# Kernel tuning notes

Hardware: AMD Instinct MI355X
Metric: run time of the kernel (lower is better)

The kernel has to match this reference:

```python
import jax, jax.numpy as jnp
import numpy as np

C, N, E = 256, 256, 2048          # subgraphs, nodes/subgraph, edges/subgraph
F_IN, NHID, DDI = 128, 128, 256
K1, K2, K3 = 128, 64, 32          # top-k sizes for pooling_ratio=0.5
P, B = 16, 16                     # DAG hierarchy: P parents x B leaf children
GN = C + P + 1                    # global DAG nodes (leaves + parents + root)
GE = 8192                         # global pos/neg edge count


def setup_inputs():
    key = jax.random.key(0)
    ks = jax.random.split(key, 16)
    inp = {
        "x": jax.random.normal(ks[0], (C, N, F_IN), jnp.float32),
        "edge_index": jax.random.randint(ks[1], (C, 2, E), 0, N),
        "edge_weight": jax.random.uniform(ks[2], (C, E), dtype=jnp.float32),
        "global_edge_index": jax.random.randint(ks[3], (2, GE), 0, GN),
        "neg_edge_index": jax.random.randint(ks[4], (2, GE), 0, GN),
    }
    names = [("W1", F_IN, NHID), ("Wp1", NHID, 1), ("W2", NHID, NHID),
             ("Wp2", NHID, 1), ("W3", NHID, NHID), ("Wp3", NHID, 1),
             ("Wg", 6 * NHID, DDI), ("Wl1", DDI, DDI), ("Wl2", DDI, DDI)]
    for i, (nm, fi, fo) in enumerate(names):
        inp[nm] = jax.random.normal(ks[5 + i], (fi, fo), jnp.float32) / np.sqrt(fi)
        inp["b" + nm[1:]] = jnp.zeros((fo,), jnp.float32)
    return inp


def gcn(x, ei, ew, W, b):
    """PyG GCNConv with self-loops: D^-1/2 (A+I) D^-1/2 X W + b."""
    n = x.shape[0]
    h = x @ W
    row, col = ei[0], ei[1]
    deg = 1.0 + jax.ops.segment_sum(ew, col, num_segments=n)
    dis = jax.lax.rsqrt(deg)
    norm = dis[row] * ew * dis[col]                       # [E]
    agg = jax.ops.segment_sum(norm[:, None] * h[row], col, num_segments=n)
    return agg + h / deg[:, None] + b


def sag_pool(x, ei, ew, Ws, bs, k):
    """SAGPooling: GCN score, per-graph top-k, gate by tanh(score), edge filter."""
    n = x.shape[0]
    score = gcn(x, ei, ew, Ws, bs)[:, 0]
    vals, perm = jax.lax.top_k(score, k)
    x_new = x[perm] * jnp.tanh(vals)[:, None]
    newid = jnp.full((n,), -1, jnp.int32).at[perm].set(jnp.arange(k, dtype=jnp.int32))
    r, c = newid[ei[0]], newid[ei[1]]
    keep = (r >= 0) & (c >= 0)
    ei_new = jnp.where(keep, jnp.stack([r, c]), 0)        # dropped edges -> node 0
    ew_new = jnp.where(keep, ew, 0.0)                     # with zero weight
    return x_new, ei_new, ew_new


def _subgraph(x, ei, ew, W1, b1, Wp1, bp1, W2, b2, Wp2, bp2, W3, b3, Wp3, bp3):
    x = jax.nn.relu(gcn(x, ei, ew, W1, b1))
    x, ei, ew = sag_pool(x, ei, ew, Wp1, bp1, K1)
    x1 = jnp.concatenate([x.max(0), x.mean(0)])           # gmp||gap, batch all-zero
    x = jax.nn.relu(gcn(x, ei, ew, W2, b2))
    x, ei, ew = sag_pool(x, ei, ew, Wp2, bp2, K2)
    x2 = jnp.concatenate([x.max(0), x.mean(0)])
    x = jax.nn.relu(gcn(x, ei, ew, W3, b3))
    x, ei, ew = sag_pool(x, ei, ew, Wp3, bp3, K3)
    x3 = jnp.concatenate([x.max(0), x.mean(0)])
    return jnp.concatenate([x1, x2, x3])                  # [6*NHID]


def reference(x, edge_index, edge_weight, global_edge_index, neg_edge_index,
              W1, b1, Wp1, bp1, W2, b2, Wp2, bp2, W3, b3, Wp3, bp3,
              Wg, bg, Wl1, bl1, Wl2, bl2):
    # per-class subgraph pipeline, vmapped over the C subgraphs
    leaf = jax.vmap(_subgraph, in_axes=(0, 0, 0) + (None,) * 12)(
        x, edge_index, edge_weight,
        W1, b1, Wp1, bp1, W2, b2, Wp2, bp2, W3, b3, Wp3, bp3)   # [C, 6*NHID]
    # Get_Fs: mean-aggregate children features up the DAG (fixed 2-level + root)
    parent = leaf.reshape(P, B, -1).mean(axis=1)                # [P, 6*NHID]
    root = parent.mean(axis=0, keepdims=True)                   # [1, 6*NHID]
    gfeat = jnp.concatenate([leaf, parent, root], axis=0)       # [GN, 6*NHID]
    # global GCN (unit edge weights)
    gx = jax.nn.relu(gcn(gfeat, global_edge_index,
                         jnp.ones((GE,), gfeat.dtype), Wg, bg)) # [GN, DDI]
    class_embedding = gx[:C]
    # feature_split + lin1/lin2 + dot-product scores
    pos_s = gx[global_edge_index[0]] @ Wl1 + bl1
    pos_t = gx[global_edge_index[1]] @ Wl2 + bl2
    neg_s = gx[neg_edge_index[0]] @ Wl1 + bl1
    neg_t = gx[neg_edge_index[1]] @ Wl2 + bl2
    pos = jnp.sum(pos_s * pos_t, axis=1)
    neg = jnp.sum(neg_s * neg_t, axis=1)
    # BCEWithLogits: targets 1 for pos, 0 for neg
    loss = jnp.mean(jax.nn.softplus(-pos)) + jnp.mean(jax.nn.softplus(neg))
    return class_embedding, loss
```

## Files before the change

kernel.cpp:

```cpp
#include <hip/hip_runtime.h>
#include <math.h>

#define NT 1024
#define EDGES 2048
#define SENT 0xFFFF

struct SmemA {
  float xbuf[256 * 128];
  unsigned short rc[EDGES];
  float ewl[EDGES];
  unsigned short csr_row[EDGES];
  float csr_coef[EDGES];
  float degs[256];
  float diss[256];
  int   csr_off[257];
  int   csr_cnt[256];
  float hsv[256];
  float scorev[256];
  float vals[128];
  short perm[128];
  signed char newid[256];
};

__device__ __forceinline__ float4* xvec(float* xb, int row, int c4) {
  return reinterpret_cast<float4*>(xb + (row << 7) + ((c4 ^ (row & 7)) << 2));
}
__device__ __forceinline__ int xidx(int row, int col) {
  return (row << 7) + ((((col >> 2) ^ (row & 7)) << 2) | (col & 3));
}

template<int NN, int K, bool FIRST, bool REMAP>
__device__ __forceinline__ void run_stage(
    SmemA& sm,
    const float* __restrict__ xg,
    const int* __restrict__ eic,
    const float* __restrict__ ewc,
    const float* __restrict__ W,
    const float* __restrict__ b,
    const float* __restrict__ Wp,
    const float* __restrict__ bp,
    float* __restrict__ leaf_out,
    float& lmax, float& lmean)
{
  constexpr int NPT  = NN / 64;
  constexpr int Q    = NN / 64;
  constexpr int SEG  = NT / NN;
  constexpr int LEN  = NN / SEG;
  constexpr int LOG  = (NN == 256) ? 8 : (NN == 128 ? 7 : 6);
  const int tid  = threadIdx.x;
  const int lane = tid & 63;
  const int fbase = __builtin_amdgcn_readfirstlane((tid >> 6) << 3);
  const int c4b   = fbase >> 2;

  if (FIRST) {
    if (tid < NN) { sm.degs[tid] = 1.0f; sm.csr_cnt[tid] = 0; }
    __syncthreads();
    const float4* xg4 = reinterpret_cast<const float4*>(xg);
    for (int i = tid; i < 256 * 32; i += NT) {
      const float4 v = xg4[i];
      *xvec(sm.xbuf, i >> 5, i & 31) = v;
    }
    for (int e = tid; e < EDGES; e += NT) {
      const int row = eic[e], col = eic[EDGES + e];
      const float w = ewc[e];
      sm.rc[e]  = (unsigned short)((row << 8) | col);
      sm.ewl[e] = w;
      atomicAdd(&sm.degs[col], w);
      atomicAdd(&sm.csr_cnt[col], 1);
    }
    __syncthreads();
  }

  if (tid < NN) sm.diss[tid] = rsqrtf(sm.degs[tid]);
  if (tid < 64) {
    int c[Q], pre[Q];
    int tot = 0;
#pragma unroll
    for (int i = 0; i < Q; i++) { c[i] = sm.csr_cnt[tid * Q + i]; pre[i] = tot; tot += c[i]; }
    int inc = tot;
#pragma unroll
    for (int d = 1; d < 64; d <<= 1) {
      const int o = __shfl_up(inc, d, 64);
      if (tid >= d) inc += o;
    }
    const int base = inc - tot;
    if (tid == 0) sm.csr_off[0] = 0;
#pragma unroll
    for (int i = 0; i < Q; i++) {
      sm.csr_off[tid * Q + i + 1] = base + pre[i] + c[i];
      sm.csr_cnt[tid * Q + i] = 0;
    }
  }
  __syncthreads();

  if (tid < NN) sm.hsv[tid] = 0.0f;
  for (int e = tid; e < EDGES; e += NT) {
    const unsigned short r = sm.rc[e];
    if (FIRST || r != SENT) {
      const int row = r >> 8, col = r & 255;
      const int p = atomicAdd(&sm.csr_cnt[col], 1);
      const int s = sm.csr_off[col] + p;
      sm.csr_row[s]  = (unsigned short)row;
      sm.csr_coef[s] = sm.diss[row] * sm.ewl[e];
    }
  }
  __syncthreads();

  float acc[NPT][8];
#pragma unroll
  for (int i = 0; i < NPT; i++)
#pragma unroll
    for (int j = 0; j < 8; j++) acc[i][j] = 0.0f;

#pragma unroll 4
  for (int k4 = 0; k4 < 32; k4++) {
    float4 xv[NPT];
#pragma unroll
    for (int i = 0; i < NPT; i++) xv[i] = *xvec(sm.xbuf, lane + (i << 6), k4);
#pragma unroll
    for (int kk = 0; kk < 4; kk++) {
      const float* wr = W + (((k4 << 2) + kk) << 7) + fbase;
      const float4 wa = *reinterpret_cast<const float4*>(wr);
      const float4 wb = *reinterpret_cast<const float4*>(wr + 4);
      const float wv[8] = {wa.x, wa.y, wa.z, wa.w, wb.x, wb.y, wb.z, wb.w};
#pragma unroll
      for (int i = 0; i < NPT; i++) {
        const float xs = (kk == 0) ? xv[i].x : (kk == 1) ? xv[i].y : (kk == 2) ? xv[i].z : xv[i].w;
#pragma unroll
        for (int j = 0; j < 8; j++) acc[i][j] = fmaf(xs, wv[j], acc[i][j]);
      }
    }
  }
  __syncthreads();

#pragma unroll
  for (int i = 0; i < NPT; i++) {
    const int v = lane + (i << 6);
    *xvec(sm.xbuf, v, c4b)     = make_float4(acc[i][0], acc[i][1], acc[i][2], acc[i][3]);
    *xvec(sm.xbuf, v, c4b + 1) = make_float4(acc[i][4], acc[i][5], acc[i][6], acc[i][7]);
  }
  __syncthreads();

  {
    const float4 ba = *reinterpret_cast<const float4*>(b + fbase);
    const float4 bb = *reinterpret_cast<const float4*>(b + fbase + 4);
    const float bv[8] = {ba.x, ba.y, ba.z, ba.w, bb.x, bb.y, bb.z, bb.w};
    const float4 wa = *reinterpret_cast<const float4*>(Wp + fbase);
    const float4 wb = *reinterpret_cast<const float4*>(Wp + fbase + 4);
    const float wv[8] = {wa.x, wa.y, wa.z, wa.w, wb.x, wb.y, wb.z, wb.w};
#pragma unroll
    for (int i = 0; i < NPT; i++) {
      const int v = lane + (i << 6);
      const int beg = sm.csr_off[v], end = sm.csr_off[v + 1];
      float ag[8] = {0.f, 0.f, 0.f, 0.f, 0.f, 0.f, 0.f, 0.f};
      float4 plo = make_float4(0.f, 0.f, 0.f, 0.f), phi = plo;
      float cf_nxt = 0.0f;
      if (beg < end) {
        const int r0 = sm.csr_row[beg];
        cf_nxt = sm.csr_coef[beg];
        plo = *xvec(sm.xbuf, r0, c4b);
        phi = *xvec(sm.xbuf, r0, c4b + 1);
      }
      for (int s = beg; s < end; ++s) {
        const float4 lo = plo, hi = phi;
        const float cf = cf_nxt;
        if (s + 1 < end) {
          const int rn = sm.csr_row[s + 1];
          cf_nxt = sm.csr_coef[s + 1];
          plo = *xvec(sm.xbuf, rn, c4b);
          phi = *xvec(sm.xbuf, rn, c4b + 1);
        }
        ag[0] = fmaf(cf, lo.x, ag[0]); ag[1] = fmaf(cf, lo.y, ag[1]);
        ag[2] = fmaf(cf, lo.z, ag[2]); ag[3] = fmaf(cf, lo.w, ag[3]);
        ag[4] = fmaf(cf, hi.x, ag[4]); ag[5] = fmaf(cf, hi.y, ag[5]);
        ag[6] = fmaf(cf, hi.z, ag[6]); ag[7] = fmaf(cf, hi.w, ag[7]);
      }
      const float dv = sm.diss[v];
      const float invd = 1.0f / sm.degs[v];
      float part = 0.0f;
#pragma unroll
      for (int j = 0; j < 8; j++) {
        acc[i][j] = fmaxf(fmaf(ag[j], dv, fmaf(acc[i][j], invd, bv[j])), 0.0f);
        part = fmaf(acc[i][j], wv[j], part);
      }
      atomicAdd(&sm.hsv[v], part);
    }
  }
  __syncthreads();

#pragma unroll
  for (int i = 0; i < NPT; i++) {
    const int v = lane + (i << 6);
    *xvec(sm.xbuf, v, c4b)     = make_float4(acc[i][0], acc[i][1], acc[i][2], acc[i][3]);
    *xvec(sm.xbuf, v, c4b + 1) = make_float4(acc[i][4], acc[i][5], acc[i][6], acc[i][7]);
  }
  if (tid < NN) {
    const int v = tid;
    const int beg = sm.csr_off[v], end = sm.csr_off[v + 1];
    float s = 0.0f;
    int r_nxt = 0; float c_nxt = 0.0f;
    if (beg < end) { r_nxt = sm.csr_row[beg]; c_nxt = sm.csr_coef[beg]; }
    for (int e2 = beg; e2 < end; e2++) {
      const int r = r_nxt; const float cf = c_nxt;
      if (e2 + 1 < end) { r_nxt = sm.csr_row[e2 + 1]; c_nxt = sm.csr_coef[e2 + 1]; }
      s = fmaf(cf, sm.hsv[r], s);
    }
    sm.scorev[v] = s * sm.diss[v] + sm.hsv[v] / sm.degs[v] + bp[0];
    sm.csr_cnt[v] = 0;
  }
  __syncthreads();

  {
    const int node = tid & (NN - 1);
    const int seg  = tid >> LOG;
    const float sv = sm.scorev[node];
    int part = 0;
    const int u0 = seg * LEN;
#pragma unroll 4
    for (int u = u0; u < u0 + LEN; u++) {
      const float su = sm.scorev[u];
      part += (su > sv) || (su == sv && u < node);
    }
    if (part) atomicAdd(&sm.csr_cnt[node], part);
  }
  __syncthreads();
  if (tid < NN) {
    const int rank = sm.csr_cnt[tid];
    if (rank < K) { sm.perm[rank] = (short)tid; sm.vals[rank] = sm.scorev[tid]; sm.newid[tid] = (signed char)rank; }
    else sm.newid[tid] = -1;
    if (tid < K) { sm.degs[tid] = 1.0f; sm.csr_cnt[tid] = 0; }
  }
  __syncthreads();

  {
    constexpr int TPR = NT / K;
    constexpr int C4  = 32 / TPR;
    const int drow = tid / TPR;
    const int cc   = (tid % TPR) * C4;
    const int src  = sm.perm[drow];
    const float g  = tanhf(sm.vals[drow]);
    float4 tmp[C4];
#pragma unroll
    for (int j = 0; j < C4; j++) tmp[j] = *xvec(sm.xbuf, src, cc + j);
    __syncthreads();
#pragma unroll
    for (int j = 0; j < C4; j++) {
      tmp[j].x *= g; tmp[j].y *= g; tmp[j].z *= g; tmp[j].w *= g;
      *xvec(sm.xbuf, drow, cc + j) = tmp[j];
    }
  }
  __syncthreads();

  if (tid < 128) {
    float mx = -INFINITY, sv = 0.0f;
    for (int i = 0; i < K; i++) {
      const float v = sm.xbuf[xidx(i, tid)];
      mx = fmaxf(mx, v); sv += v;
    }
    lmax = mx;
    lmean = sv * (1.0f / K);
    leaf_out[tid] = mx;
    leaf_out[128 + tid] = lmean;
  }
  if (REMAP) {
    for (int e = tid; e < EDGES; e += NT) {
      const unsigned short r = sm.rc[e];
      if (FIRST || r != SENT) {
        const int r2 = sm.newid[r >> 8];
        const int c2 = sm.newid[r & 255];
        if (r2 < 0 || c2 < 0) sm.rc[e] = SENT;
        else {
          sm.rc[e] = (unsigned short)((r2 << 8) | c2);
          atomicAdd(&sm.degs[c2], sm.ewl[e]);
          atomicAdd(&sm.csr_cnt[c2], 1);
        }
      }
    }
  }
  __syncthreads();
}

__global__ __launch_bounds__(NT)
void stageA_kernel(const float* __restrict__ x0,
                   const int* __restrict__ ei, const float* __restrict__ ew,
                   const float* __restrict__ W1, const float* __restrict__ b1,
                   const float* __restrict__ Wp1, const float* __restrict__ bp1,
                   const float* __restrict__ W2, const float* __restrict__ b2,
                   const float* __restrict__ Wp2, const float* __restrict__ bp2,
                   const float* __restrict__ W3, const float* __restrict__ b3,
                   const float* __restrict__ Wp3, const float* __restrict__ bp3,
                   const float* __restrict__ Wg,
                   float* __restrict__ gfeat, float* __restrict__ hG)
{
  __shared__ SmemA sm;
  const int c = blockIdx.x;
  const int tid = threadIdx.x;
  if (c == 0 && tid < 256) hG[(size_t)272 * 256 + tid] = 0.0f;
  const int* eic = ei + (size_t)c * 2 * EDGES;
  const float* ewc = ew + (size_t)c * EDGES;
  const float* xgc = x0 + (size_t)c * 256 * 128;
  float* leaf = gfeat + (size_t)c * 768;
  float l0 = 0.f, l1 = 0.f, l2 = 0.f, l3 = 0.f, l4 = 0.f, l5 = 0.f;
  run_stage<256, 128, true,  true >(sm, xgc, eic, ewc, W1, b1, Wp1, bp1, leaf + 0,   l0, l1);
  run_stage<128,  64, false, true >(sm, nullptr, nullptr, nullptr, W2, b2, Wp2, bp2, leaf + 256, l2, l3);
  run_stage< 64,  32, false, false>(sm, nullptr, nullptr, nullptr, W3, b3, Wp3, bp3, leaf + 512, l4, l5);

  float* leafbuf = sm.csr_coef;
  float* hGacc   = sm.degs;
  if (tid < 256) {
    if (tid < 128) {
      leafbuf[tid]       = l0; leafbuf[128 + tid] = l1;
      leafbuf[256 + tid] = l2; leafbuf[384 + tid] = l3;
      leafbuf[512 + tid] = l4; leafbuf[640 + tid] = l5;
    }
    hGacc[tid] = 0.0f;
  }
  __syncthreads();
  {
    const int f = tid & 255, q = tid >> 8;
    const float* wgq = Wg + (size_t)(q * 192) * 256 + f;
    const float* lb  = leafbuf + q * 192;
    float p0 = 0.f, p1 = 0.f, p2 = 0.f, p3 = 0.f;
    for (int i = 0; i < 192; i += 4) {
      p0 = fmaf(lb[i],     wgq[(size_t)i * 256],       p0);
      p1 = fmaf(lb[i + 1], wgq[(size_t)(i + 1) * 256], p1);
      p2 = fmaf(lb[i + 2], wgq[(size_t)(i + 2) * 256], p2);
      p3 = fmaf(lb[i + 3], wgq[(size_t)(i + 3) * 256], p3);
    }
    atomicAdd(&hGacc[f], (p0 + p1) + (p2 + p3));
  }
  __syncthreads();
  if (tid < 256) hG[(size_t)c * 256 + tid] = hGacc[tid];
}

__global__ __launch_bounds__(NT)
void prep_k(const float* __restrict__ gfeat, const float* __restrict__ Wg,
            float* __restrict__ hG, const int* __restrict__ gei,
            float* __restrict__ degG, int* __restrict__ goff,
            int* __restrict__ gcsr_row, float* __restrict__ gcsr_coef,
            float* __restrict__ lacc, int* __restrict__ lctr) {
  const int tid = threadIdx.x;
  if (blockIdx.x == 16) {
    __shared__ int cnt[320];
    __shared__ int off[321];
    __shared__ int fc[288];
    for (int i = tid; i < 320; i += NT) cnt[i] = 0;
    if (tid < 288) fc[tid] = 0;
    __syncthreads();
    for (int e = tid; e < 8192; e += NT) atomicAdd(&cnt[gei[8192 + e]], 1);
    __syncthreads();
    if (tid < 64) {
      int c[5], pre[5];
      int tot = 0;
#pragma unroll
      for (int i = 0; i < 5; i++) { c[i] = cnt[tid * 5 + i]; pre[i] = tot; tot += c[i]; }
      int inc = tot;
#pragma unroll
      for (int d = 1; d < 64; d <<= 1) {
        const int o = __shfl_up(inc, d, 64);
        if (tid >= d) inc += o;
      }
      const int base = inc - tot;
      if (tid == 0) off[0] = 0;
#pragma unroll
      for (int i = 0; i < 5; i++) off[tid * 5 + i + 1] = base + pre[i] + c[i];
    }
    if (tid < 273) degG[tid] = 1.0f + (float)cnt[tid];
    __syncthreads();
    for (int e = tid; e < 8192; e += NT) {
      const int col = gei[8192 + e], row = gei[e];
      const int p = atomicAdd(&fc[col], 1);
      const int s = off[col] + p;
      gcsr_row[s]  = row;
      gcsr_coef[s] = rsqrtf(1.0f + (float)cnt[row]);
    }
    if (tid < 274) goff[tid] = off[tid];
    if (tid == 0) { *lacc = 0.0f; *lctr = 0; }
    return;
  }
  const int p = blockIdx.x;
  __shared__ float prow[768];
  __shared__ float hGacc[256];
  for (int k = tid; k < 768; k += NT) {
    float s0 = 0.f, s1 = 0.f;
#pragma unroll
    for (int b2 = 0; b2 < 16; b2 += 2) {
      s0 += gfeat[(size_t)(p * 16 + b2) * 768 + k];
      s1 += gfeat[(size_t)(p * 16 + b2 + 1) * 768 + k];
    }
    prow[k] = (s0 + s1) * (1.0f / 16.0f);
  }
  if (tid < 256) hGacc[tid] = 0.0f;
  __syncthreads();
  {
    const int f = tid & 255, q = tid >> 8;
    const float* wgq = Wg + (size_t)(q * 192) * 256 + f;
    const float* lb  = prow + q * 192;
    float p0 = 0.f, p1 = 0.f, p2 = 0.f, p3 = 0.f;
    for (int i = 0; i < 192; i += 4) {
      p0 = fmaf(lb[i],     wgq[(size_t)i * 256],       p0);
      p1 = fmaf(lb[i + 1], wgq[(size_t)(i + 1) * 256], p1);
      p2 = fmaf(lb[i + 2], wgq[(size_t)(i + 2) * 256], p2);
      p3 = fmaf(lb[i + 3], wgq[(size_t)(i + 3) * 256], p3);
    }
    atomicAdd(&hGacc[f], (p0 + p1) + (p2 + p3));
  }
  __syncthreads();
  if (tid < 256) {
    const float hv = hGacc[tid];
    hG[(size_t)(256 + p) * 256 + tid] = hv;
    atomicAdd(&hG[(size_t)272 * 256 + tid], hv * (1.0f / 16.0f));
  }
}

__global__ __launch_bounds__(NT)
void gaggemb_k(const float* __restrict__ hG, const float* __restrict__ degG,
               const int* __restrict__ goff, const int* __restrict__ gcsr_row,
               const float* __restrict__ gcsr_coef, const float* __restrict__ bg,
               const float* __restrict__ Wl1, const float* __restrict__ bl1,
               const float* __restrict__ Wl2, const float* __restrict__ bl2,
               float* __restrict__ out_ce, float* __restrict__ A,
               float* __restrict__ B) {
  __shared__ float pacc[1024];
  __shared__ float pacc2[1024];
  __shared__ float gxr[256];
  const int v = blockIdx.x, tid = threadIdx.x;
  const int f = tid & 255, q = tid >> 8;
  const int beg = goff[v], end = goff[v + 1];
  float s = 0.f;
  for (int i = beg + q; i < end; i += 4)
    s = fmaf(gcsr_coef[i], hG[(size_t)gcsr_row[i] * 256 + f], s);
  pacc[tid] = s;
  __syncthreads();
  if (tid < 256) {
    const float dg = degG[v];
    float val = (pacc[tid] + pacc[256 + tid] + pacc[512 + tid] + pacc[768 + tid]) * rsqrtf(dg)
              + hG[(size_t)v * 256 + tid] / dg + bg[tid];
    val = fmaxf(val, 0.0f);
    gxr[tid] = val;
    if (v < 256) out_ce[(size_t)v * 256 + tid] = val;
  }
  __syncthreads();
  {
    const int k0 = q << 6;
    float a = 0.f, b2 = 0.f;
    for (int k = k0; k < k0 + 64; k++) {
      const float g = gxr[k];
      a  = fmaf(g, Wl1[(size_t)k * 256 + f], a);
      b2 = fmaf(g, Wl2[(size_t)k * 256 + f], b2);
    }
    pacc[tid] = a; pacc2[tid] = b2;
  }
  __syncthreads();
  if (tid < 256) {
    A[(size_t)v * 256 + tid] = pacc[tid] + pacc[256 + tid] + pacc[512 + tid] + pacc[768 + tid] + bl1[tid];
    B[(size_t)v * 256 + tid] = pacc2[tid] + pacc2[256 + tid] + pacc2[512 + tid] + pacc2[768 + tid] + bl2[tid];
  }
}

__global__ __launch_bounds__(256)
void loss_k(const float* __restrict__ A, const float* __restrict__ B,
            const int* __restrict__ gei, const int* __restrict__ nei,
            float* __restrict__ acc, int* __restrict__ lctr,
            float* __restrict__ out) {
  const int gw = (blockIdx.x * blockDim.x + threadIdx.x) >> 6;
  const int lane = threadIdx.x & 63;
  float lsum = 0.0f;
  for (int idx = gw; idx < 16384; idx += 512) {
    const bool ispos = idx < 8192;
    const int e = ispos ? idx : idx - 8192;
    const int* ia = ispos ? gei : nei;
    const int s = ia[e], t = ia[8192 + e];
    float p = 0.0f;
#pragma unroll
    for (int j = 0; j < 4; j++)
      p += A[(size_t)s * 256 + lane + 64 * j] * B[(size_t)t * 256 + lane + 64 * j];
#pragma unroll
    for (int off = 32; off; off >>= 1) p += __shfl_xor(p, off, 64);
    const float z = ispos ? -p : p;
    lsum += fmaxf(z, 0.0f) + log1pf(expf(-fabsf(z)));
  }
  if (lane == 0) atomicAdd(acc, lsum);
  __syncthreads();
  if (threadIdx.x == 0) {
    __threadfence();
    const int old = atomicAdd(lctr, 1);
    if (old == (int)gridDim.x - 1) {
      const float tot = atomicAdd(acc, 0.0f);
      out[65536] = tot * (1.0f / 8192.0f);
    }
  }
}

extern "C" void kernel_launch(void* const* d_in, const int* in_sizes, int n_in,
                              void* d_out, int out_size, void* d_ws, size_t ws_size,
                              hipStream_t stream) {
  const float* x   = (const float*)d_in[0];
  const int*   ei  = (const int*)d_in[1];
  const float* ew  = (const float*)d_in[2];
  const int*   gei = (const int*)d_in[3];
  const int*   nei = (const int*)d_in[4];
  const float* W1  = (const float*)d_in[5];
  const float* b1  = (const float*)d_in[6];
  const float* Wp1 = (const float*)d_in[7];
  const float* bp1 = (const float*)d_in[8];
  const float* W2  = (const float*)d_in[9];
  const float* b2  = (const float*)d_in[10];
  const float* Wp2 = (const float*)d_in[11];
  const float* bp2 = (const float*)d_in[12];
  const float* W3  = (const float*)d_in[13];
  const float* b3  = (const float*)d_in[14];
  const float* Wp3 = (const float*)d_in[15];
  const float* bp3 = (const float*)d_in[16];
  const float* Wg  = (const float*)d_in[17];
  const float* bg  = (const float*)d_in[18];
  const float* Wl1 = (const float*)d_in[19];
  const float* bl1 = (const float*)d_in[20];
  const float* Wl2 = (const float*)d_in[21];
  const float* bl2 = (const float*)d_in[22];

  float* ws       = (float*)d_ws;
  float* gfeat    = ws;
  float* hG       = gfeat + 256 * 768;
  float* degG     = hG + 273 * 256;
  float* Aemb     = degG + 288;
  float* Bemb     = Aemb + 273 * 256;
  float* lacc     = Bemb + 273 * 256;
  int*   lctr     = (int*)(lacc + 1);
  int*   goff     = lctr + 1;
  int*   gcsr_row = goff + 288;
  float* gcsr_coef= (float*)(gcsr_row + 8192);
  float* out      = (float*)d_out;

  stageA_kernel<<<256, NT, 0, stream>>>(x, ei, ew, W1, b1, Wp1, bp1,
                                        W2, b2, Wp2, bp2, W3, b3, Wp3, bp3,
                                        Wg, gfeat, hG);
  prep_k<<<17, NT, 0, stream>>>(gfeat, Wg, hG, gei, degG, goff,
                                gcsr_row, gcsr_coef, lacc, lctr);
  gaggemb_k<<<273, NT, 0, stream>>>(hG, degG, goff, gcsr_row, gcsr_coef, bg,
                                    Wl1, bl1, Wl2, bl2, out, Aemb, Bemb);
  loss_k<<<128, 256, 0, stream>>>(Aemb, Bemb, gei, nei, lacc, lctr, out);
}
```

Measured before the change: 185.8 us.

## Fuse global GCN tail into one cooperative kernel and compute parents from hG

```diff
diff --git a/kernel.cpp b/kernel.cpp
--- a/kernel.cpp
+++ b/kernel.cpp
@@ -1,9 +1,12 @@
 #include <hip/hip_runtime.h>
+#include <hip/hip_cooperative_groups.h>
 #include <math.h>
 
 #define NT 1024
 #define EDGES 2048
 #define SENT 0xFFFF
+
+namespace cg = cooperative_groups;
 
 struct SmemA {
   float xbuf[256 * 128];
@@ -39,7 +42,6 @@
     const float* __restrict__ b,
     const float* __restrict__ Wp,
     const float* __restrict__ bp,
-    float* __restrict__ leaf_out,
     float& lmax, float& lmean)
 {
   constexpr int NPT  = NN / 64;
@@ -93,7 +95,7 @@
   }
   __syncthreads();
 
-  if (tid < NN) sm.hsv[tid] = 0.0f;
+  if (tid < NN) { sm.hsv[tid] = 0.0f; sm.scorev[tid] = 0.0f; }
   for (int e = tid; e < EDGES; e += NT) {
     const unsigned short r = sm.rc[e];
     if (FIRST || r != SENT) {
@@ -194,19 +196,17 @@
     *xvec(sm.xbuf, v, c4b)     = make_float4(acc[i][0], acc[i][1], acc[i][2], acc[i][3]);
     *xvec(sm.xbuf, v, c4b + 1) = make_float4(acc[i][4], acc[i][5], acc[i][6], acc[i][7]);
   }
+  for (int e = tid; e < EDGES; e += NT) {
+    const unsigned short r = sm.rc[e];
+    if (FIRST || r != SENT) {
+      const int row = r >> 8, col = r & 255;
+      atomicAdd(&sm.scorev[col], sm.diss[row] * sm.ewl[e] * sm.hsv[row]);
+    }
+  }
+  __syncthreads();
   if (tid < NN) {
-    const int v = tid;
-    const int beg = sm.csr_off[v], end = sm.csr_off[v + 1];
-    float s = 0.0f;
-    int r_nxt = 0; float c_nxt = 0.0f;
-    if (beg < end) { r_nxt = sm.csr_row[beg]; c_nxt = sm.csr_coef[beg]; }
-    for (int e2 = beg; e2 < end; e2++) {
-      const int r = r_nxt; const float cf = c_nxt;
-      if (e2 + 1 < end) { r_nxt = sm.csr_row[e2 + 1]; c_nxt = sm.csr_coef[e2 + 1]; }
-      s = fmaf(cf, sm.hsv[r], s);
-    }
-    sm.scorev[v] = s * sm.diss[v] + sm.hsv[v] / sm.degs[v] + bp[0];
-    sm.csr_cnt[v] = 0;
+    sm.scorev[tid] = sm.scorev[tid] * sm.diss[tid] + sm.hsv[tid] / sm.degs[tid] + bp[0];
+    sm.csr_cnt[tid] = 0;
   }
   __syncthreads();
 
@@ -259,8 +259,6 @@
     }
     lmax = mx;
     lmean = sv * (1.0f / K);
-    leaf_out[tid] = mx;
-    leaf_out[128 + tid] = lmean;
   }
   if (REMAP) {
     for (int e = tid; e < EDGES; e += NT) {
@@ -289,21 +287,18 @@
                    const float* __restrict__ Wp2, const float* __restrict__ bp2,
                    const float* __restrict__ W3, const float* __restrict__ b3,
                    const float* __restrict__ Wp3, const float* __restrict__ bp3,
-                   const float* __restrict__ Wg,
-                   float* __restrict__ gfeat, float* __restrict__ hG)
+                   const float* __restrict__ Wg, float* __restrict__ hG)
 {
   __shared__ SmemA sm;
   const int c = blockIdx.x;
   const int tid = threadIdx.x;
-  if (c == 0 && tid < 256) hG[(size_t)272 * 256 + tid] = 0.0f;
   const int* eic = ei + (size_t)c * 2 * EDGES;
   const float* ewc = ew + (size_t)c * EDGES;
   const float* xgc = x0 + (size_t)c * 256 * 128;
-  float* leaf = gfeat + (size_t)c * 768;
   float l0 = 0.f, l1 = 0.f, l2 = 0.f, l3 = 0.f, l4 = 0.f, l5 = 0.f;
-  run_stage<256, 128, true,  true >(sm, xgc, eic, ewc, W1, b1, Wp1, bp1, leaf + 0,   l0, l1);
-  run_stage<128,  64, false, true >(sm, nullptr, nullptr, nullptr, W2, b2, Wp2, bp2, leaf + 256, l2, l3);
-  run_stage< 64,  32, false, false>(sm, nullptr, nullptr, nullptr, W3, b3, Wp3, bp3, leaf + 512, l4, l5);
+  run_stage<256, 128, true,  true >(sm, xgc, eic, ewc, W1, b1, Wp1, bp1, l0, l1);
+  run_stage<128,  64, false, true >(sm, nullptr, nullptr, nullptr, W2, b2, Wp2, bp2, l2, l3);
+  run_stage< 64,  32, false, false>(sm, nullptr, nullptr, nullptr, W3, b3, Wp3, bp3, l4, l5);
 
   float* leafbuf = sm.csr_coef;
   float* hGacc   = sm.degs;
@@ -333,27 +328,56 @@
   if (tid < 256) hG[(size_t)c * 256 + tid] = hGacc[tid];
 }
 
-__global__ __launch_bounds__(NT)
-void prep_k(const float* __restrict__ gfeat, const float* __restrict__ Wg,
-            float* __restrict__ hG, const int* __restrict__ gei,
+struct TailSm {
+  float pacc[1024];
+  float pacc2[1024];
+  float gxr[256];
+};
+
+__global__ __launch_bounds__(NT, 1)
+void tail_k(float* __restrict__ hG, const int* __restrict__ gei,
+            const int* __restrict__ nei, const float* __restrict__ bg,
+            const float* __restrict__ Wl1, const float* __restrict__ bl1,
+            const float* __restrict__ Wl2, const float* __restrict__ bl2,
             float* __restrict__ degG, int* __restrict__ goff,
             int* __restrict__ gcsr_row, float* __restrict__ gcsr_coef,
-            float* __restrict__ lacc, int* __restrict__ lctr) {
-  const int tid = threadIdx.x;
-  if (blockIdx.x == 16) {
-    __shared__ int cnt[320];
-    __shared__ int off[321];
-    __shared__ int fc[288];
+            float* __restrict__ A, float* __restrict__ B,
+            float* __restrict__ lacc, int* __restrict__ lctr,
+            float* __restrict__ out)
+{
+  __shared__ TailSm ts;
+  cg::grid_group grid = cg::this_grid();
+  const int c = blockIdx.x, tid = threadIdx.x;
+
+  if (c == 0) {
+    for (int w = tid; w < 16 * 256; w += NT) {
+      const int p = w >> 8, f = w & 255;
+      float s = 0.f;
+#pragma unroll
+      for (int b2 = 0; b2 < 16; b2++) s += hG[(size_t)(p * 16 + b2) * 256 + f];
+      hG[(size_t)(256 + p) * 256 + f] = s * (1.0f / 16.0f);
+    }
+    __syncthreads();
+    if (tid < 256) {
+      float s = 0.f;
+#pragma unroll
+      for (int p = 0; p < 16; p++) s += hG[(size_t)(256 + p) * 256 + tid];
+      hG[(size_t)272 * 256 + tid] = s * (1.0f / 16.0f);
+    }
+  } else if (c == 1) {
+    int* cnt = (int*)ts.pacc;
+    int* off = (int*)ts.pacc + 320;
+    int* fc  = (int*)ts.pacc + 644;
     for (int i = tid; i < 320; i += NT) cnt[i] = 0;
     if (tid < 288) fc[tid] = 0;
     __syncthreads();
     for (int e = tid; e < 8192; e += NT) atomicAdd(&cnt[gei[8192 + e]], 1);
     __syncthreads();
     if (tid < 64) {
-      int c[5], pre[5];
+      int cc[5], pre[5];
       int tot = 0;
 #pragma unroll
-      for (int i = 0; i < 5; i++) { c[i] = cnt[tid * 5 + i]; pre[i] = tot; tot += c[i]; }
+      for (int i = 0; i < 5; i++) { cc[i] = cnt[tid * 5 + i]; pre[i] = tot; tot += cc[i]; }
       int inc = tot;
 #pragma unroll
       for (int d = 1; d < 64; d <<= 1) {
@@ -363,7 +387,7 @@
       const int base = inc - tot;
       if (tid == 0) off[0] = 0;
 #pragma unroll
-      for (int i = 0; i < 5; i++) off[tid * 5 + i + 1] = base + pre[i] + c[i];
+      for (int i = 0; i < 5; i++) off[tid * 5 + i + 1] = base + pre[i] + cc[i];
     }
     if (tid < 273) degG[tid] = 1.0f + (float)cnt[tid];
     __syncthreads();
@@ -376,118 +400,79 @@
     }
     if (tid < 274) goff[tid] = off[tid];
     if (tid == 0) { *lacc = 0.0f; *lctr = 0; }
-    return;
-  }
-  const int p = blockIdx.x;
-  __shared__ float prow[768];
-  __shared__ float hGacc[256];
-  for (int k = tid; k < 768; k += NT) {
-    float s0 = 0.f, s1 = 0.f;
-#pragma unroll
-    for (int b2 = 0; b2 < 16; b2 += 2) {
-      s0 += gfeat[(size_t)(p * 16 + b2) * 768 + k];
-      s1 += gfeat[(size_t)(p * 16 + b2 + 1) * 768 + k];
-    }
-    prow[k] = (s0 + s1) * (1.0f / 16.0f);
-  }
-  if (tid < 256) hGacc[tid] = 0.0f;
-  __syncthreads();
+  }
+  grid.sync();
+
+  for (int rr = 0; rr < 2; rr++) {
+    if (rr == 1 && c >= 17) break;
+    const int v = rr ? 256 + c : c;
+    const int f = tid & 255, q = tid >> 8;
+    const int beg = goff[v], end = goff[v + 1];
+    float s = 0.f;
+    for (int i = beg + q; i < end; i += 4)
+      s = fmaf(gcsr_coef[i], hG[(size_t)gcsr_row[i] * 256 + f], s);
+    ts.pacc[tid] = s;
+    __syncthreads();
+    if (tid < 256) {
+      const float dg = degG[v];
+      float val = (ts.pacc[tid] + ts.pacc[256 + tid] + ts.pacc[512 + tid] + ts.pacc[768 + tid]) * rsqrtf(dg)
+                + hG[(size_t)v * 256 + tid] / dg + bg[tid];
+      val = fmaxf(val, 0.0f);
+      ts.gxr[tid] = val;
+      if (v < 256) out[(size_t)v * 256 + tid] = val;
+    }
+    __syncthreads();
+    {
+      const int k0 = q << 6;
+      float a = 0.f, b2 = 0.f;
+      for (int k = k0; k < k0 + 64; k++) {
+        const float g = ts.gxr[k];
+        a  = fmaf(g, Wl1[(size_t)k * 256 + f], a);
+        b2 = fmaf(g, Wl2[(size_t)k * 256 + f], b2);
+      }
+      ts.pacc[tid] = a; ts.pacc2[tid] = b2;
+    }
+    __syncthreads();
+    if (tid < 256) {
+      A[(size_t)v * 256 + tid] = ts.pacc[tid] + ts.pacc[256 + tid] + ts.pacc[512 + tid] + ts.pacc[768 + tid] + bl1[tid];
+      B[(size_t)v * 256 + tid] = ts.pacc2[tid] + ts.pacc2[256 + tid] + ts.pacc2[512 + tid] + ts.pacc2[768 + tid] + bl2[tid];
+    }
+    __syncthreads();
+  }
+  grid.sync();
+
   {
-    const int f = tid & 255, q = tid >> 8;
-    const float* wgq = Wg + (size_t)(q * 192) * 256 + f;
-    const float* lb  = prow + q * 192;
-    float p0 = 0.f, p1 = 0.f, p2 = 0.f, p3 = 0.f;
-    for (int i = 0; i < 192; i += 4) {
-      p0 = fmaf(lb[i],     wgq[(size_t)i * 256],       p0);
-      p1 = fmaf(lb[i + 1], wgq[(size_t)(i + 1) * 256], p1);
-      p2 = fmaf(lb[i + 2], wgq[(size_t)(i + 2) * 256], p2);
-      p3 = fmaf(lb[i + 3], wgq[(size_t)(i + 3) * 256], p3);
-    }
-    atomicAdd(&hGacc[f], (p0 + p1) + (p2 + p3));
-  }
-  __syncthreads();
-  if (tid < 256) {
-    const float hv = hGacc[tid];
-    hG[(size_t)(256 + p) * 256 + tid] = hv;
-    atomicAdd(&hG[(size_t)272 * 256 + tid], hv * (1.0f / 16.0f));
-  }
-}
-
-__global__ __launch_bounds__(NT)
-void gaggemb_k(const float* __restrict__ hG, const float* __restrict__ degG,
-               const int* __restrict__ goff, const int* __restrict__ gcsr_row,
-               const float* __restrict__ gcsr_coef, const float* __restrict__ bg,
-               const float* __restrict__ Wl1, const float* __restrict__ bl1,
-               const float* __restrict__ Wl2, const float* __restrict__ bl2,
-               float* __restrict__ out_ce, float* __restrict__ A,
-               float* __restrict__ B) {
-  __shared__ float pacc[1024];
-  __shared__ float pacc2[1024];
-  __shared__ float gxr[256];
-  const int v = blockIdx.x, tid = threadIdx.x;
-  const int f = tid & 255, q = tid >> 8;
-  const int beg = goff[v], end = goff[v + 1];
-  float s = 0.f;
-  for (int i = beg + q; i < end; i += 4)
-    s = fmaf(gcsr_coef[i], hG[(size_t)gcsr_row[i] * 256 + f], s);
-  pacc[tid] = s;
-  __syncthreads();
-  if (tid < 256) {
-    const float dg = degG[v];
-    float val = (pacc[tid] + pacc[256 + tid] + pacc[512 + tid] + pacc[768 + tid]) * rsqrtf(dg)
-              + hG[(size_t)v * 256 + tid] / dg + bg[tid];
-    val = fmaxf(val, 0.0f);
-    gxr[tid] = val;
-    if (v < 256) out_ce[(size_t)v * 256 + tid] = val;
-  }
-  __syncthreads();
-  {
-    const int k0 = q << 6;
-    float a = 0.f, b2 = 0.f;
-    for (int k = k0; k < k0 + 64; k++) {
-      const float g = gxr[k];
-      a  = fmaf(g, Wl1[(size_t)k * 256 + f], a);
-      b2 = fmaf(g, Wl2[(size_t)k * 256 + f], b2);
-    }
-    pacc[tid] = a; pacc2[tid] = b2;
-  }
-  __syncthreads();
-  if (tid < 256) {
-    A[(size_t)v * 256 + tid] = pacc[tid] + pacc[256 + tid] + pacc[512 + tid] + pacc[768 + tid] + bl1[tid];
-    B[(size_t)v * 256 + tid] = pacc2[tid] + pacc2[256 + tid] + pacc2[512 + tid] + pacc2[768 + tid] + bl2[tid];
-  }
-}
-
-__global__ __launch_bounds__(256)
-void loss_k(const float* __restrict__ A, const float* __restrict__ B,
-            const int* __restrict__ gei, const int* __restrict__ nei,
-            float* __restrict__ acc, int* __restrict__ lctr,
-            float* __restrict__ out) {
-  const int gw = (blockIdx.x * blockDim.x + threadIdx.x) >> 6;
-  const int lane = threadIdx.x & 63;
-  float lsum = 0.0f;
-  for (int idx = gw; idx < 16384; idx += 512) {
-    const bool ispos = idx < 8192;
-    const int e = ispos ? idx : idx - 8192;
-    const int* ia = ispos ? gei : nei;
-    const int s = ia[e], t = ia[8192 + e];
-    float p = 0.0f;
-#pragma unroll
-    for (int j = 0; j < 4; j++)
-      p += A[(size_t)s * 256 + lane + 64 * j] * B[(size_t)t * 256 + lane + 64 * j];
-#pragma unroll
-    for (int off = 32; off; off >>= 1) p += __shfl_xor(p, off, 64);
-    const float z = ispos ? -p : p;
-    lsum += fmaxf(z, 0.0f) + log1pf(expf(-fabsf(z)));
-  }
-  if (lane == 0) atomicAdd(acc, lsum);
-  __syncthreads();
-  if (threadIdx.x == 0) {
-    __threadfence();
-    const int old = atomicAdd(lctr, 1);
-    if (old == (int)gridDim.x - 1) {
-      const float tot = atomicAdd(acc, 0.0f);
-      out[65536] = tot * (1.0f / 8192.0f);
+    if (tid == 0) ts.pacc[0] = 0.0f;
+    __syncthreads();
+    const int gw16 = (c << 4) + (tid >> 6);
+    const int lane = tid & 63;
+    float lsum = 0.0f;
+#pragma unroll
+    for (int j = 0; j < 4; j++) {
+      const int idx = (gw16 << 2) + j;
+      const bool ispos = idx < 8192;
+      const int e = idx & 8191;
+      const int* ia = ispos ? gei : nei;
+      const int s2 = ia[e], t2 = ia[8192 + e];
+      float p = 0.0f;
+#pragma unroll
+      for (int m = 0; m < 4; m++)
+        p += A[(size_t)s2 * 256 + lane + (m << 6)] * B[(size_t)t2 * 256 + lane + (m << 6)];
+#pragma unroll
+      for (int off = 32; off; off >>= 1) p += __shfl_xor(p, off, 64);
+      const float z = ispos ? -p : p;
+      lsum += fmaxf(z, 0.0f) + log1pf(expf(-fabsf(z)));
+    }
+    if (lane == 0) atomicAdd(&ts.pacc[0], lsum);
+    __syncthreads();
+    if (tid == 0) {
+      atomicAdd(lacc, ts.pacc[0]);
+      __threadfence();
+      const int old = atomicAdd(lctr, 1);
+      if (old == 255) {
+        const float tot = atomicAdd(lacc, 0.0f);
+        out[65536] = tot * (1.0f / 8192.0f);
+      }
     }
   }
 }
@@ -520,8 +505,7 @@
   const float* bl2 = (const float*)d_in[22];
 
   float* ws       = (float*)d_ws;
-  float* gfeat    = ws;
-  float* hG       = gfeat + 256 * 768;
+  float* hG       = ws;
   float* degG     = hG + 273 * 256;
   float* Aemb     = degG + 288;
   float* Bemb     = Aemb + 273 * 256;
@@ -534,10 +518,12 @@
 
   stageA_kernel<<<256, NT, 0, stream>>>(x, ei, ew, W1, b1, Wp1, bp1,
                                         W2, b2, Wp2, bp2, W3, b3, Wp3, bp3,
-                                        Wg, gfeat, hG);
-  prep_k<<<17, NT, 0, stream>>>(gfeat, Wg, hG, gei, degG, goff,
-                                gcsr_row, gcsr_coef, lacc, lctr);
-  gaggemb_k<<<273, NT, 0, stream>>>(hG, degG, goff, gcsr_row, gcsr_coef, bg,
-                                    Wl1, bl1, Wl2, bl2, out, Aemb, Bemb);
-  loss_k<<<128, 256, 0, stream>>>(Aemb, Bemb, gei, nei, lacc, lctr, out);
+                                        Wg, hG);
+  void* targs[] = {
+    (void*)&hG, (void*)&gei, (void*)&nei, (void*)&bg,
+    (void*)&Wl1, (void*)&bl1, (void*)&Wl2, (void*)&bl2,
+    (void*)&degG, (void*)&goff, (void*)&gcsr_row, (void*)&gcsr_coef,
+    (void*)&Aemb, (void*)&Bemb, (void*)&lacc, (void*)&lctr, (void*)&out
+  };
+  hipLaunchCooperativeKernel((const void*)tail_k, dim3(256), dim3(NT), targs, 0, stream);
 }
```

Result: slower. 323.8 us (+74.3%).

## Fuse prep kernel into stageA via extra block and completion counter

Applied to the files above, without the earlier changes.

```diff
diff --git a/kernel.cpp b/kernel.cpp
--- a/kernel.cpp
+++ b/kernel.cpp
@@ -39,7 +39,6 @@
     const float* __restrict__ b,
     const float* __restrict__ Wp,
     const float* __restrict__ bp,
-    float* __restrict__ leaf_out,
     float& lmax, float& lmean)
 {
   constexpr int NPT  = NN / 64;
@@ -93,7 +92,7 @@
   }
   __syncthreads();
 
-  if (tid < NN) sm.hsv[tid] = 0.0f;
+  if (tid < NN) { sm.hsv[tid] = 0.0f; sm.scorev[tid] = 0.0f; }
   for (int e = tid; e < EDGES; e += NT) {
     const unsigned short r = sm.rc[e];
     if (FIRST || r != SENT) {
@@ -194,19 +193,17 @@
     *xvec(sm.xbuf, v, c4b)     = make_float4(acc[i][0], acc[i][1], acc[i][2], acc[i][3]);
     *xvec(sm.xbuf, v, c4b + 1) = make_float4(acc[i][4], acc[i][5], acc[i][6], acc[i][7]);
   }
+  for (int e = tid; e < EDGES; e += NT) {
+    const unsigned short r = sm.rc[e];
+    if (FIRST || r != SENT) {
+      const int row = r >> 8, col = r & 255;
+      atomicAdd(&sm.scorev[col], sm.diss[row] * sm.ewl[e] * sm.hsv[row]);
+    }
+  }
+  __syncthreads();
   if (tid < NN) {
-    const int v = tid;
-    const int beg = sm.csr_off[v], end = sm.csr_off[v + 1];
-    float s = 0.0f;
-    int r_nxt = 0; float c_nxt = 0.0f;
-    if (beg < end) { r_nxt = sm.csr_row[beg]; c_nxt = sm.csr_coef[beg]; }
-    for (int e2 = beg; e2 < end; e2++) {
-      const int r = r_nxt; const float cf = c_nxt;
-      if (e2 + 1 < end) { r_nxt = sm.csr_row[e2 + 1]; c_nxt = sm.csr_coef[e2 + 1]; }
-      s = fmaf(cf, sm.hsv[r], s);
-    }
-    sm.scorev[v] = s * sm.diss[v] + sm.hsv[v] / sm.degs[v] + bp[0];
-    sm.csr_cnt[v] = 0;
+    sm.scorev[tid] = sm.scorev[tid] * sm.diss[tid] + sm.hsv[tid] / sm.degs[tid] + bp[0];
+    sm.csr_cnt[tid] = 0;
   }
   __syncthreads();
 
@@ -259,8 +256,6 @@
     }
     lmax = mx;
     lmean = sv * (1.0f / K);
-    leaf_out[tid] = mx;
-    leaf_out[128 + tid] = lmean;
   }
   if (REMAP) {
     for (int e = tid; e < EDGES; e += NT) {
@@ -283,27 +278,90 @@
 __global__ __launch_bounds__(NT)
 void stageA_kernel(const float* __restrict__ x0,
                    const int* __restrict__ ei, const float* __restrict__ ew,
+                   const int* __restrict__ gei,
                    const float* __restrict__ W1, const float* __restrict__ b1,
                    const float* __restrict__ Wp1, const float* __restrict__ bp1,
                    const float* __restrict__ W2, const float* __restrict__ b2,
                    const float* __restrict__ Wp2, const float* __restrict__ bp2,
                    const float* __restrict__ W3, const float* __restrict__ b3,
                    const float* __restrict__ Wp3, const float* __restrict__ bp3,
-                   const float* __restrict__ Wg,
-                   float* __restrict__ gfeat, float* __restrict__ hG)
+                   const float* __restrict__ Wg, float* __restrict__ hG,
+                   float* __restrict__ degG, int* __restrict__ goff,
+                   int* __restrict__ gcsr_row, float* __restrict__ gcsr_coef,
+                   float* __restrict__ lacc, int* __restrict__ lctr,
+                   int* __restrict__ pctr)
 {
   __shared__ SmemA sm;
   const int c = blockIdx.x;
   const int tid = threadIdx.x;
-  if (c == 0 && tid < 256) hG[(size_t)272 * 256 + tid] = 0.0f;
+
+  if (c == 256) {
+    int* cnt = (int*)sm.xbuf;
+    int* off = cnt + 320;
+    int* fc  = off + 321;
+    for (int i = tid; i < 320; i += NT) cnt[i] = 0;
+    if (tid < 288) fc[tid] = 0;
+    __syncthreads();
+    for (int e = tid; e < 8192; e += NT) atomicAdd(&cnt[gei[8192 + e]], 1);
+    __syncthreads();
+    if (tid < 64) {
+      int cc[5], pre[5];
+      int tot = 0;
+#pragma unroll
+      for (int i = 0; i < 5; i++) { cc[i] = cnt[tid * 5 + i]; pre[i] = tot; tot += cc[i]; }
+      int inc = tot;
+#pragma unroll
+      for (int d = 1; d < 64; d <<= 1) {
+        const int o = __shfl_up(inc, d, 64);
+        if (tid >= d) inc += o;
+      }
+      const int base = inc - tot;
+      if (tid == 0) off[0] = 0;
+#pragma unroll
+      for (int i = 0; i < 5; i++) off[tid * 5 + i + 1] = base + pre[i] + cc[i];
+    }
+    if (tid < 273) degG[tid] = 1.0f + (float)cnt[tid];
+    __syncthreads();
+    for (int e = tid; e < 8192; e += NT) {
+      const int col = gei[8192 + e], row = gei[e];
+      const int p = atomicAdd(&fc[col], 1);
+      const int s = off[col] + p;
+      gcsr_row[s]  = row;
+      gcsr_coef[s] = rsqrtf(1.0f + (float)cnt[row]);
+    }
+    if (tid < 274) goff[tid] = off[tid];
+    if (tid == 0) { *lacc = 0.0f; *lctr = 0; }
+
+    if (tid == 0) {
+      while (__hip_atomic_load(pctr, __ATOMIC_ACQUIRE, __HIP_MEMORY_SCOPE_AGENT) < 256)
+        __builtin_amdgcn_s_sleep(8);
+    }
+    __syncthreads();
+    __threadfence();
+
+    float* racc = sm.hsv;
+    if (tid < 256) racc[tid] = 0.0f;
+    __syncthreads();
+    for (int w = tid; w < 16 * 256; w += NT) {
+      const int p = w >> 8, f = w & 255;
+      float s = 0.f;
+#pragma unroll 4
+      for (int b2 = 0; b2 < 16; b2++) s += hG[(size_t)(p * 16 + b2) * 256 + f];
+      hG[(size_t)(256 + p) * 256 + f] = s * (1.0f / 16.0f);
+      atomicAdd(&racc[f], s * (1.0f / 256.0f));
+    }
+    __syncthreads();
+    if (tid < 256) hG[(size_t)272 * 256 + tid] = racc[tid];
+    return;
+  }
+
   const int* eic = ei + (size_t)c * 2 * EDGES;
   const float* ewc = ew + (size_t)c * EDGES;
   const float* xgc = x0 + (size_t)c * 256 * 128;
-  float* leaf = gfeat + (size_t)c * 768;
   float l0 = 0.f, l1 = 0.f, l2 = 0.f, l3 = 0.f, l4 = 0.f, l5 = 0.f;
-  run_stage<256, 128, true,  true >(sm, xgc, eic, ewc, W1, b1, Wp1, bp1, leaf + 0,   l0, l1);
-  run_stage<128,  64, false, true >(sm, nullptr, nullptr, nullptr, W2, b2, Wp2, bp2, leaf + 256, l2, l3);
-  run_stage< 64,  32, false, false>(sm, nullptr, nullptr, nullptr, W3, b3, Wp3, bp3, leaf + 512, l4, l5);
+  run_stage<256, 128, true,  true >(sm, xgc, eic, ewc, W1, b1, Wp1, bp1, l0, l1);
+  run_stage<128,  64, false, true >(sm, nullptr, nullptr, nullptr, W2, b2, Wp2, bp2, l2, l3);
+  run_stage< 64,  32, false, false>(sm, nullptr, nullptr, nullptr, W3, b3, Wp3, bp3, l4, l5);
 
   float* leafbuf = sm.csr_coef;
   float* hGacc   = sm.degs;
@@ -331,85 +389,11 @@
   }
   __syncthreads();
   if (tid < 256) hG[(size_t)c * 256 + tid] = hGacc[tid];
-}
-
-__global__ __launch_bounds__(NT)
-void prep_k(const float* __restrict__ gfeat, const float* __restrict__ Wg,
-            float* __restrict__ hG, const int* __restrict__ gei,
-            float* __restrict__ degG, int* __restrict__ goff,
-            int* __restrict__ gcsr_row, float* __restrict__ gcsr_coef,
-            float* __restrict__ lacc, int* __restrict__ lctr) {
-  const int tid = threadIdx.x;
-  if (blockIdx.x == 16) {
-    __shared__ int cnt[320];
-    __shared__ int off[321];
-    __shared__ int fc[288];
-    for (int i = tid; i < 320; i += NT) cnt[i] = 0;
-    if (tid < 288) fc[tid] = 0;
-    __syncthreads();
-    for (int e = tid; e < 8192; e += NT) atomicAdd(&cnt[gei[8192 + e]], 1);
-    __syncthreads();
-    if (tid < 64) {
-      int c[5], pre[5];
-      int tot = 0;
-#pragma unroll
-      for (int i = 0; i < 5; i++) { c[i] = cnt[tid * 5 + i]; pre[i] = tot; tot += c[i]; }
-      int inc = tot;
-#pragma unroll
-      for (int d = 1; d < 64; d <<= 1) {
-        const int o = __shfl_up(inc, d, 64);
-        if (tid >= d) inc += o;
-      }
-      const int base = inc - tot;
-      if (tid == 0) off[0] = 0;
-#pragma unroll
-      for (int i = 0; i < 5; i++) off[tid * 5 + i + 1] = base + pre[i] + c[i];
-    }
-    if (tid < 273) degG[tid] = 1.0f + (float)cnt[tid];
-    __syncthreads();
-    for (int e = tid; e < 8192; e += NT) {
-      const int col = gei[8192 + e], row = gei[e];
-      const int p = atomicAdd(&fc[col], 1);
-      const int s = off[col] + p;
-      gcsr_row[s]  = row;
-      gcsr_coef[s] = rsqrtf(1.0f + (float)cnt[row]);
-    }
-    if (tid < 274) goff[tid] = off[tid];
-    if (tid == 0) { *lacc = 0.0f; *lctr = 0; }
-    return;
-  }
-  const int p = blockIdx.x;
-  __shared__ float prow[768];
-  __shared__ float hGacc[256];
-  for (int k = tid; k < 768; k += NT) {
-    float s0 = 0.f, s1 = 0.f;
-#pragma unroll
-    for (int b2 = 0; b2 < 16; b2 += 2) {
-      s0 += gfeat[(size_t)(p * 16 + b2) * 768 + k];
-      s1 += gfeat[(size_t)(p * 16 + b2 + 1) * 768 + k];
-    }
-    prow[k] = (s0 + s1) * (1.0f / 16.0f);
-  }
-  if (tid < 256) hGacc[tid] = 0.0f;
-  __syncthreads();
-  {
-    const int f = tid & 255, q = tid >> 8;
-    const float* wgq = Wg + (size_t)(q * 192) * 256 + f;
-    const float* lb  = prow + q * 192;
-    float p0 = 0.f, p1 = 0.f, p2 = 0.f, p3 = 0.f;
-    for (int i = 0; i < 192; i += 4) {
-      p0 = fmaf(lb[i],     wgq[(size_t)i * 256],       p0);
-      p1 = fmaf(lb[i + 1], wgq[(size_t)(i + 1) * 256], p1);
-      p2 = fmaf(lb[i + 2], wgq[(size_t)(i + 2) * 256], p2);
-      p3 = fmaf(lb[i + 3], wgq[(size_t)(i + 3) * 256], p3);
-    }
-    atomicAdd(&hGacc[f], (p0 + p1) + (p2 + p3));
-  }
-  __syncthreads();
-  if (tid < 256) {
-    const float hv = hGacc[tid];
-    hG[(size_t)(256 + p) * 256 + tid] = hv;
-    atomicAdd(&hG[(size_t)272 * 256 + tid], hv * (1.0f / 16.0f));
+
+  __syncthreads();
+  if (tid == 0) {
+    __threadfence();
+    __hip_atomic_fetch_add(pctr, 1, __ATOMIC_RELEASE, __HIP_MEMORY_SCOPE_AGENT);
   }
 }
 
@@ -520,23 +504,23 @@
   const float* bl2 = (const float*)d_in[22];
 
   float* ws       = (float*)d_ws;
-  float* gfeat    = ws;
-  float* hG       = gfeat + 256 * 768;
+  float* hG       = ws;
   float* degG     = hG + 273 * 256;
   float* Aemb     = degG + 288;
   float* Bemb     = Aemb + 273 * 256;
   float* lacc     = Bemb + 273 * 256;
   int*   lctr     = (int*)(lacc + 1);
-  int*   goff     = lctr + 1;
+  int*   pctr     = lctr + 1;
+  int*   goff     = pctr + 1;
   int*   gcsr_row = goff + 288;
   float* gcsr_coef= (float*)(gcsr_row + 8192);
   float* out      = (float*)d_out;
 
-  stageA_kernel<<<256, NT, 0, stream>>>(x, ei, ew, W1, b1, Wp1, bp1,
+  hipMemsetAsync(pctr, 0, sizeof(int), stream);
+  stageA_kernel<<<257, NT, 0, stream>>>(x, ei, ew, gei, W1, b1, Wp1, bp1,
                                         W2, b2, Wp2, bp2, W3, b3, Wp3, bp3,
-                                        Wg, gfeat, hG);
-  prep_k<<<17, NT, 0, stream>>>(gfeat, Wg, hG, gei, degG, goff,
-                                gcsr_row, gcsr_coef, lacc, lctr);
+                                        Wg, hG, degG, goff, gcsr_row, gcsr_coef,
+                                        lacc, lctr, pctr);
   gaggemb_k<<<273, NT, 0, stream>>>(hG, degG, goff, gcsr_row, gcsr_coef, bg,
                                     Wl1, bl1, Wl2, bl2, out, Aemb, Bemb);
   loss_k<<<128, 256, 0, stream>>>(Aemb, Bemb, gei, nei, lacc, lctr, out);
```

Measured after the change: 207.3 us. +11.6%, slower.
